# Kernel tuning notes

Hardware: AMD Instinct MI355X
Metric: run time of the kernel (lower is better)

The kernel has to match this reference:

```python
import jax, jax.numpy as jnp
import numpy as np

THRESH = 0.5
MARGIN = 0.1
SCALE_POS = 2.0
SCALE_NEG = 40.0
EPSILON = 1e-5


def setup_inputs() -> dict:
    key = jax.random.key(0)
    kx, kl = jax.random.split(key)
    B, D, N_CLASSES = 4096, 1024, 256
    x = jax.random.normal(kx, (B, D), dtype=jnp.float32)
    # L2-normalize embeddings (standard for multi-similarity loss; keeps sim in [-1, 1])
    x = x / jnp.linalg.norm(x, axis=1, keepdims=True)
    labels = jax.random.randint(kl, (B,), 0, N_CLASSES, dtype=jnp.int64)
    return {"x": x, "labels": labels}


def reference(x, labels):
    B = x.shape[0]
    sim = jnp.matmul(x, x.T)  # [B, B]

    eye = jnp.eye(B, dtype=bool)
    same = labels[:, None] == labels[None, :]
    pos_mask = same & ~eye                      # positives excl. self
    neg_mask = ~same                            # negatives
    pos_valid = pos_mask & (sim < 1.0 - EPSILON)  # pos_pair_ after < 1-eps filter

    # per-row hardest stats (inf/-inf where empty)
    min_pos = jnp.min(jnp.where(pos_valid, sim, jnp.inf), axis=1)   # min over pos_pair_
    max_neg = jnp.max(jnp.where(neg_mask, sim, -jnp.inf), axis=1)   # max over neg_pair_

    # mined pairs
    neg_keep = neg_mask & (sim + MARGIN > min_pos[:, None])
    pos_keep = pos_valid & (sim - MARGIN < max_neg[:, None])

    has_row = (pos_valid.any(axis=1) & neg_mask.any(axis=1)
               & pos_keep.any(axis=1) & neg_keep.any(axis=1))

    pos_sum = jnp.sum(jnp.where(pos_keep, jnp.exp(-SCALE_POS * (sim - THRESH)), 0.0), axis=1)
    neg_sum = jnp.sum(jnp.where(neg_keep, jnp.exp(SCALE_NEG * (sim - THRESH)), 0.0), axis=1)

    pos_loss = jnp.log1p(pos_sum) / SCALE_POS
    neg_loss = jnp.log1p(neg_sum) / SCALE_NEG

    row_loss = jnp.where(has_row, pos_loss + neg_loss, 0.0)
    return jnp.sum(row_loss) / B
```

## Files before the change

kernel.cpp:

```cpp
#include <hip/hip_runtime.h>
#include <hip/hip_bf16.h>
#include <math.h>
#include <stdint.h>


#define THRESH    0.5f
#define MARGIN    0.1f
#define SCALE_POS 2.0f
#define SCALE_NEG 40.0f
#define POS_CAP   (1.0f - 1e-5f)

typedef __bf16 bf16x8 __attribute__((ext_vector_type(8)));
typedef float  f32x4  __attribute__((ext_vector_type(4)));

__device__ __forceinline__ uint16_t f2bf(float f) {
  union { float f; uint32_t u; } v; v.f = f;
  uint32_t u = v.u;
  u += 0x7FFFu + ((u >> 16) & 1u);
  return (uint16_t)(u >> 16);
}

__device__ __forceinline__ uint32_t fenc(float f) {
  union { float f; uint32_t u; } v; v.f = f;
  return (v.u & 0x80000000u) ? ~v.u : (v.u ^ 0x80000000u);
}
__device__ __forceinline__ float fdec(uint32_t k) {
  union { float f; uint32_t u; } v;
  v.u = (k & 0x80000000u) ? (k ^ 0x80000000u) : ~k;
  return v.f;
}

__global__ __launch_bounds__(256) void cvt_bf16_kernel(
    const float* __restrict__ x, uint16_t* __restrict__ y, int n) {
  int i = (blockIdx.x * 256 + threadIdx.x) * 4;
  if (i + 3 < n) {
    float4 v = *(const float4*)(x + i);
    ushort4 o;
    o.x = f2bf(v.x); o.y = f2bf(v.y); o.z = f2bf(v.z); o.w = f2bf(v.w);
    *(ushort4*)(y + i) = o;
  }
}

#if defined(__has_builtin)
#if __has_builtin(__builtin_amdgcn_global_load_lds)
#define HAVE_GLL 1
#endif
#endif

__device__ __forceinline__ void stage16(const uint16_t* g, uint16_t* lds_wave_base, int lane) {
#ifdef HAVE_GLL
  __builtin_amdgcn_global_load_lds(
      (const __attribute__((address_space(1))) void*)g,
      (__attribute__((address_space(3))) void*)lds_wave_base, 16, 0, 0);
#else
  *(uint4*)(lds_wave_base + lane * 8) = *(const uint4*)g;
#endif
}

__global__ __launch_bounds__(256) void simgemm_kernel(
    const uint16_t* __restrict__ X, const int* __restrict__ labels,
    float* __restrict__ C, uint32_t* __restrict__ gmin, uint32_t* __restrict__ gmax,
    int B, int D) {
  __shared__ __align__(16) uint16_t sT[2][2][128 * 64];
  __shared__ int slabR[128];
  __shared__ int slabC[128];

  const int nblk = B >> 7;
  const int nb   = nblk * (nblk + 1) / 2;

  int t = blockIdx.x;
  if ((nb & 7) == 0) {
    const int cpx = nb >> 3;
    t = (t % 8) * cpx + t / 8;
  }
  int bi = 0;
  while (t >= nblk - bi) { t -= nblk - bi; ++bi; }
  const int bj = bi + t;
  const int bm = bi * 128;
  const int bn = bj * 128;

  const int tid  = threadIdx.x;
  const int wave = tid >> 6;
  const int lane = tid & 63;
  const int waveM = wave >> 1, waveN = wave & 1;

  if (tid < 128) slabR[tid] = labels[bm + tid];
  else           slabC[tid - 128] = labels[bn + tid - 128];

  const uint16_t* gA = X + (size_t)bm * D;
  const uint16_t* gB = X + (size_t)bn * D;

  int srcOff[4];
#pragma unroll
  for (int s = 0; s < 4; ++s) {
    const int idx = s * 256 + tid;
    const int row = idx >> 3;
    const int cb  = ((idx & 7) << 4) ^ ((row & 7) << 4);
    srcOff[s] = row * D + (cb >> 1);
  }

  const int fr = lane & 15;
  const int fq = lane >> 4;
  const int sw = (fr & 7) << 4;

  f32x4 acc[4][4] = {};

  const int NT = D >> 6;

#pragma unroll
  for (int s = 0; s < 4; ++s) {
    uint16_t* dA = &sT[0][0][0] + (s * 256 + wave * 64) * 8;
    uint16_t* dB = &sT[0][1][0] + (s * 256 + wave * 64) * 8;
    stage16(gA + srcOff[s], dA, lane);
    stage16(gB + srcOff[s], dB, lane);
  }
  __syncthreads();

  int cur = 0;
  for (int kt = 0; kt < NT; ++kt) {
    if (kt + 1 < NT) {
      const int k0 = (kt + 1) << 6;
#pragma unroll
      for (int s = 0; s < 4; ++s) {
        uint16_t* dA = &sT[cur ^ 1][0][0] + (s * 256 + wave * 64) * 8;
        uint16_t* dB = &sT[cur ^ 1][1][0] + (s * 256 + wave * 64) * 8;
        stage16(gA + srcOff[s] + k0, dA, lane);
        stage16(gB + srcOff[s] + k0, dB, lane);
      }
    }

    const char* tA = (const char*)&sT[cur][0][0];
    const char* tB = (const char*)&sT[cur][1][0];
#pragma unroll
    for (int kk = 0; kk < 2; ++kk) {
      const int cbyte = (kk * 64 + fq * 16) ^ sw;
      bf16x8 af[4], bfv[4];
#pragma unroll
      for (int mt = 0; mt < 4; ++mt) {
        const int rowa = waveM * 64 + mt * 16 + fr;
        af[mt] = *(const bf16x8*)(tA + rowa * 128 + cbyte);
      }
#pragma unroll
      for (int nt = 0; nt < 4; ++nt) {
        const int rowb = waveN * 64 + nt * 16 + fr;
        bfv[nt] = *(const bf16x8*)(tB + rowb * 128 + cbyte);
      }
#pragma unroll
      for (int mt = 0; mt < 4; ++mt)
#pragma unroll
        for (int nt = 0; nt < 4; ++nt)
          acc[mt][nt] = __builtin_amdgcn_mfma_f32_16x16x32_bf16(
              af[mt], bfv[nt], acc[mt][nt], 0, 0, 0);
    }

    __syncthreads();
    cur ^= 1;
  }

#pragma unroll
  for (int mt = 0; mt < 4; ++mt) {
#pragma unroll
    for (int nt = 0; nt < 4; ++nt) {
      const int col = bn + waveN * 64 + nt * 16 + fr;
#pragma unroll
      for (int r = 0; r < 4; ++r) {
        const int row = bm + waveM * 64 + mt * 16 + fq * 4 + r;
        C[(size_t)row * B + col] = acc[mt][nt][r];
      }
    }
  }

  if (bi != bj) {
#pragma unroll
    for (int mt = 0; mt < 4; ++mt) {
#pragma unroll
      for (int nt = 0; nt < 4; ++nt) {
        const int col  = bn + waveN * 64 + nt * 16 + fr;
        const int rowb = bm + waveM * 64 + mt * 16 + fq * 4;
        *(f32x4*)(C + (size_t)col * B + rowb) = acc[mt][nt];
      }
    }
  }

  const float INF = __builtin_inff();

  int lr[4][4];
#pragma unroll
  for (int mt = 0; mt < 4; ++mt)
#pragma unroll
    for (int r = 0; r < 4; ++r)
      lr[mt][r] = slabR[waveM * 64 + mt * 16 + fq * 4 + r];
  int lc[4];
#pragma unroll
  for (int nt = 0; nt < 4; ++nt) lc[nt] = slabC[waveN * 64 + nt * 16 + fr];

  {
    float rmin[4][4], rmax[4][4];
#pragma unroll
    for (int mt = 0; mt < 4; ++mt)
#pragma unroll
      for (int r = 0; r < 4; ++r) { rmin[mt][r] = INF; rmax[mt][r] = -INF; }

#pragma unroll
    for (int mt = 0; mt < 4; ++mt) {
#pragma unroll
      for (int nt = 0; nt < 4; ++nt) {
        const int gcol = bn + waveN * 64 + nt * 16 + fr;
#pragma unroll
        for (int r = 0; r < 4; ++r) {
          const int grow = bm + waveM * 64 + mt * 16 + fq * 4 + r;
          const float s = acc[mt][nt][r];
          if (lr[mt][r] == lc[nt]) {
            if (grow != gcol && s < POS_CAP) rmin[mt][r] = fminf(rmin[mt][r], s);
          } else {
            rmax[mt][r] = fmaxf(rmax[mt][r], s);
          }
        }
      }
    }
#pragma unroll
    for (int mt = 0; mt < 4; ++mt)
#pragma unroll
      for (int r = 0; r < 4; ++r) {
#pragma unroll
        for (int m = 1; m < 16; m <<= 1) {
          rmin[mt][r] = fminf(rmin[mt][r], __shfl_xor(rmin[mt][r], m, 64));
          rmax[mt][r] = fmaxf(rmax[mt][r], __shfl_xor(rmax[mt][r], m, 64));
        }
      }
    if (fr == 0) {
#pragma unroll
      for (int mt = 0; mt < 4; ++mt)
#pragma unroll
        for (int r = 0; r < 4; ++r) {
          const int grow = bm + waveM * 64 + mt * 16 + fq * 4 + r;
          if (rmin[mt][r] < INF)  atomicMin(&gmin[grow], fenc(rmin[mt][r]));
          if (rmax[mt][r] > -INF) atomicMax(&gmax[grow], fenc(rmax[mt][r]));
        }
    }
  }

  if (bi != bj) {
    float cmin[4], cmax[4];
#pragma unroll
    for (int nt = 0; nt < 4; ++nt) { cmin[nt] = INF; cmax[nt] = -INF; }

#pragma unroll
    for (int nt = 0; nt < 4; ++nt) {
      const int gcol = bn + waveN * 64 + nt * 16 + fr;
#pragma unroll
      for (int mt = 0; mt < 4; ++mt) {
#pragma unroll
        for (int r = 0; r < 4; ++r) {
          const int grow = bm + waveM * 64 + mt * 16 + fq * 4 + r;
          const float s = acc[mt][nt][r];
          if (lc[nt] == lr[mt][r]) {
            if (grow != gcol && s < POS_CAP) cmin[nt] = fminf(cmin[nt], s);
          } else {
            cmax[nt] = fmaxf(cmax[nt], s);
          }
        }
      }
    }
#pragma unroll
    for (int nt = 0; nt < 4; ++nt) {
#pragma unroll
      for (int m = 16; m < 64; m <<= 1) {
        cmin[nt] = fminf(cmin[nt], __shfl_xor(cmin[nt], m, 64));
        cmax[nt] = fmaxf(cmax[nt], __shfl_xor(cmax[nt], m, 64));
      }
    }
    if (fq == 0) {
#pragma unroll
      for (int nt = 0; nt < 4; ++nt) {
        const int gcol = bn + waveN * 64 + nt * 16 + fr;
        if (cmin[nt] < INF)  atomicMin(&gmin[gcol], fenc(cmin[nt]));
        if (cmax[nt] > -INF) atomicMax(&gmax[gcol], fenc(cmax[nt]));
      }
    }
  }
}

__global__ __launch_bounds__(256) void rowloss_kernel(
    const float* __restrict__ sim, const int* __restrict__ labels,
    const uint32_t* __restrict__ gmin, const uint32_t* __restrict__ gmax,
    float* __restrict__ rowbuf, int B) {
  __shared__ int   slab[4096];
  __shared__ float red[8];

  const int tid  = threadIdx.x;
  const int wave = tid >> 6;
  const int lane = tid & 63;
  const float INF = __builtin_inff();

  for (int tq = tid; tq < (B >> 2); tq += 256)
    ((int4*)slab)[tq] = ((const int4*)labels)[tq];
  __syncthreads();

  const int iters = B >> 10;
  for (int rr = 0; rr < 4; ++rr) {
    const int i = blockIdx.x * 4 + rr;
    const float* row = sim + (size_t)i * B;
    const int li = slab[i];

    const uint32_t kmin = gmin[i], kmax = gmax[i];
    const bool haspos = (kmin != 0xFFFFFFFFu);
    const bool hasneg = (kmax != 0u);
    const float minpos = haspos ? fdec(kmin) : INF;
    const float maxneg = hasneg ? fdec(kmax) : -INF;

    float psum = 0.f, nsum = 0.f;
    for (int it = 0; it < iters; ++it) {
      const int j = it * 1024 + tid * 4;
      float4 v = *(const float4*)(row + j);
      float s4[4] = {v.x, v.y, v.z, v.w};
#pragma unroll
      for (int q = 0; q < 4; ++q) {
        const int jj = j + q;
        const float s = s4[q];
        if (slab[jj] == li) {
          if (jj != i && s < POS_CAP && (s - MARGIN < maxneg))
            psum += __expf(-SCALE_POS * (s - THRESH));
        } else {
          if (s + MARGIN > minpos)
            nsum += __expf(SCALE_NEG * (s - THRESH));
        }
      }
    }

#pragma unroll
    for (int m = 32; m > 0; m >>= 1) {
      psum += __shfl_xor(psum, m, 64);
      nsum += __shfl_xor(nsum, m, 64);
    }
    if (lane == 0) { red[wave] = psum; red[4 + wave] = nsum; }
    __syncthreads();

    if (tid == 0) {
      psum = red[0] + red[1] + red[2] + red[3];
      nsum = red[4] + red[5] + red[6] + red[7];
      const bool has_row = haspos && hasneg && (psum > 0.f) && (nsum > 0.f);
      rowbuf[i] = has_row
          ? (log1pf(psum) * (1.0f / SCALE_POS) + log1pf(nsum) * (1.0f / SCALE_NEG))
          : 0.f;
    }
    __syncthreads();
  }
}

__global__ __launch_bounds__(256) void finalreduce_kernel(
    const float* __restrict__ rowbuf, float* __restrict__ out, int B) {
  __shared__ float red[4];
  const int tid  = threadIdx.x;
  const int wave = tid >> 6;
  const int lane = tid & 63;

  float s = 0.f;
  for (int j = tid * 4; j < B; j += 1024) {
    float4 v = *(const float4*)(rowbuf + j);
    s += v.x + v.y + v.z + v.w;
  }
#pragma unroll
  for (int m = 32; m > 0; m >>= 1) s += __shfl_xor(s, m, 64);
  if (lane == 0) red[wave] = s;
  __syncthreads();
  if (tid == 0)
    out[0] = (red[0] + red[1] + red[2] + red[3]) * (1.0f / (float)B);
}

extern "C" void kernel_launch(void* const* d_in, const int* in_sizes, int n_in,
                              void* d_out, int out_size, void* d_ws, size_t ws_size,
                              hipStream_t stream) {
  const float* x      = (const float*)d_in[0];
  const int*   labels = (const int*)d_in[1];
  float*       out    = (float*)d_out;

  const int B = in_sizes[1];
  const int D = in_sizes[0] / B;

  uint16_t* xbf = (uint16_t*)d_ws;
  size_t xbytes = (((size_t)B * D * 2) + 255) & ~(size_t)255;
  float* sim = (float*)((char*)d_ws + xbytes);
  size_t simbytes = (size_t)B * B * 4;
  float* rowbuf = (float*)((char*)d_ws + xbytes + simbytes);
  uint32_t* gmin = (uint32_t*)((char*)d_ws + xbytes + simbytes + (size_t)B * 4);
  uint32_t* gmax = (uint32_t*)((char*)d_ws + xbytes + simbytes + (size_t)B * 8);

  hipMemsetAsync(gmin, 0xFF, (size_t)B * 4, stream);
  hipMemsetAsync(gmax, 0x00, (size_t)B * 4, stream);

  const int n = B * D;
  cvt_bf16_kernel<<<n / 1024, 256, 0, stream>>>(x, xbf, n);

  const int nblk = B / 128;
  const int nb   = nblk * (nblk + 1) / 2;
  simgemm_kernel<<<nb, 256, 0, stream>>>(xbf, labels, sim, gmin, gmax, B, D);

  rowloss_kernel<<<B / 4, 256, 0, stream>>>(sim, labels, gmin, gmax, rowbuf, B);
  finalreduce_kernel<<<1, 256, 0, stream>>>(rowbuf, out, B);
}
```

Before: 148.1 us.

## Fold memsets and final reduce into kernels, shrink GEMM K-tile, batch rowloss rows

Measured after the change: 205.4 us. 38.7% more time.

```diff
diff --git a/kernel.cpp b/kernel.cpp
--- a/kernel.cpp
+++ b/kernel.cpp
@@ -31,13 +31,23 @@
 }
 
 __global__ __launch_bounds__(256) void cvt_bf16_kernel(
-    const float* __restrict__ x, uint16_t* __restrict__ y, int n) {
-  int i = (blockIdx.x * 256 + threadIdx.x) * 4;
+    const float* __restrict__ x, uint16_t* __restrict__ y, int n,
+    uint32_t* __restrict__ gmin, uint32_t* __restrict__ gmax,
+    uint32_t* __restrict__ cnt, int B) {
+  const int tid = threadIdx.x;
+  int i = (blockIdx.x * 256 + tid) * 4;
   if (i + 3 < n) {
     float4 v = *(const float4*)(x + i);
     ushort4 o;
     o.x = f2bf(v.x); o.y = f2bf(v.y); o.z = f2bf(v.z); o.w = f2bf(v.w);
     *(ushort4*)(y + i) = o;
+  }
+  if (blockIdx.x == 0) {
+    for (int j = tid; j < B; j += 256) {
+      gmin[j] = 0xFFFFFFFFu;
+      gmax[j] = 0u;
+    }
+    if (tid == 0) *cnt = 0u;
   }
 }
 
@@ -61,7 +71,7 @@
     const uint16_t* __restrict__ X, const int* __restrict__ labels,
     float* __restrict__ C, uint32_t* __restrict__ gmin, uint32_t* __restrict__ gmax,
     int B, int D) {
-  __shared__ __align__(16) uint16_t sT[2][2][128 * 64];
+  __shared__ __align__(16) uint16_t sT[2][2][128 * 32];
   __shared__ int slabR[128];
   __shared__ int slabC[128];
 
@@ -90,25 +100,25 @@
   const uint16_t* gA = X + (size_t)bm * D;
   const uint16_t* gB = X + (size_t)bn * D;
 
-  int srcOff[4];
-#pragma unroll
-  for (int s = 0; s < 4; ++s) {
+  int srcOff[2];
+#pragma unroll
+  for (int s = 0; s < 2; ++s) {
     const int idx = s * 256 + tid;
-    const int row = idx >> 3;
-    const int cb  = ((idx & 7) << 4) ^ ((row & 7) << 4);
+    const int row = idx >> 2;
+    const int cb  = ((idx & 3) << 4) ^ ((row & 3) << 4);
     srcOff[s] = row * D + (cb >> 1);
   }
 
   const int fr = lane & 15;
   const int fq = lane >> 4;
-  const int sw = (fr & 7) << 4;
+  const int sw = (fr & 3) << 4;
 
   f32x4 acc[4][4] = {};
 
-  const int NT = D >> 6;
-
-#pragma unroll
-  for (int s = 0; s < 4; ++s) {
+  const int NT = D >> 5;
+
+#pragma unroll
+  for (int s = 0; s < 2; ++s) {
     uint16_t* dA = &sT[0][0][0] + (s * 256 + wave * 64) * 8;
     uint16_t* dB = &sT[0][1][0] + (s * 256 + wave * 64) * 8;
     stage16(gA + srcOff[s], dA, lane);
@@ -119,9 +129,9 @@
   int cur = 0;
   for (int kt = 0; kt < NT; ++kt) {
     if (kt + 1 < NT) {
-      const int k0 = (kt + 1) << 6;
-#pragma unroll
-      for (int s = 0; s < 4; ++s) {
+      const int k0 = (kt + 1) << 5;
+#pragma unroll
+      for (int s = 0; s < 2; ++s) {
         uint16_t* dA = &sT[cur ^ 1][0][0] + (s * 256 + wave * 64) * 8;
         uint16_t* dB = &sT[cur ^ 1][1][0] + (s * 256 + wave * 64) * 8;
         stage16(gA + srcOff[s] + k0, dA, lane);
@@ -131,27 +141,24 @@
 
     const char* tA = (const char*)&sT[cur][0][0];
     const char* tB = (const char*)&sT[cur][1][0];
-#pragma unroll
-    for (int kk = 0; kk < 2; ++kk) {
-      const int cbyte = (kk * 64 + fq * 16) ^ sw;
-      bf16x8 af[4], bfv[4];
-#pragma unroll
-      for (int mt = 0; mt < 4; ++mt) {
-        const int rowa = waveM * 64 + mt * 16 + fr;
-        af[mt] = *(const bf16x8*)(tA + rowa * 128 + cbyte);
-      }
-#pragma unroll
-      for (int nt = 0; nt < 4; ++nt) {
-        const int rowb = waveN * 64 + nt * 16 + fr;
-        bfv[nt] = *(const bf16x8*)(tB + rowb * 128 + cbyte);
-      }
-#pragma unroll
-      for (int mt = 0; mt < 4; ++mt)
-#pragma unroll
-        for (int nt = 0; nt < 4; ++nt)
-          acc[mt][nt] = __builtin_amdgcn_mfma_f32_16x16x32_bf16(
-              af[mt], bfv[nt], acc[mt][nt], 0, 0, 0);
-    }
+    const int cbyte = (fq * 16) ^ sw;
+    bf16x8 af[4], bfv[4];
+#pragma unroll
+    for (int mt = 0; mt < 4; ++mt) {
+      const int rowa = waveM * 64 + mt * 16 + fr;
+      af[mt] = *(const bf16x8*)(tA + rowa * 64 + cbyte);
+    }
+#pragma unroll
+    for (int nt = 0; nt < 4; ++nt) {
+      const int rowb = waveN * 64 + nt * 16 + fr;
+      bfv[nt] = *(const bf16x8*)(tB + rowb * 64 + cbyte);
+    }
+#pragma unroll
+    for (int mt = 0; mt < 4; ++mt)
+#pragma unroll
+      for (int nt = 0; nt < 4; ++nt)
+        acc[mt][nt] = __builtin_amdgcn_mfma_f32_16x16x32_bf16(
+            af[mt], bfv[nt], acc[mt][nt], 0, 0, 0);
 
     __syncthreads();
     cur ^= 1;
@@ -244,7 +251,6 @@
     float cmin[4], cmax[4];
 #pragma unroll
     for (int nt = 0; nt < 4; ++nt) { cmin[nt] = INF; cmax[nt] = -INF; }
-
 #pragma unroll
     for (int nt = 0; nt < 4; ++nt) {
       const int gcol = bn + waveN * 64 + nt * 16 + fr;
@@ -284,9 +290,12 @@
 __global__ __launch_bounds__(256) void rowloss_kernel(
     const float* __restrict__ sim, const int* __restrict__ labels,
     const uint32_t* __restrict__ gmin, const uint32_t* __restrict__ gmax,
-    float* __restrict__ rowbuf, int B) {
+    float* __restrict__ rowbuf, float* __restrict__ out,
+    uint32_t* __restrict__ cnt, int B) {
   __shared__ int   slab[4096];
-  __shared__ float red[8];
+  __shared__ float red[4][8];
+  __shared__ float fred[4];
+  __shared__ int   isLast;
 
   const int tid  = threadIdx.x;
   const int wave = tid >> 6;
@@ -297,75 +306,94 @@
     ((int4*)slab)[tq] = ((const int4*)labels)[tq];
   __syncthreads();
 
+  const int i0 = blockIdx.x * 4;
+
+  float minpos[4], maxneg[4];
+  bool  haspos[4], hasneg[4];
+  int   li[4];
+#pragma unroll
+  for (int r = 0; r < 4; ++r) {
+    const uint32_t km = gmin[i0 + r], kx = gmax[i0 + r];
+    haspos[r] = (km != 0xFFFFFFFFu);
+    hasneg[r] = (kx != 0u);
+    minpos[r] = haspos[r] ? fdec(km) : INF;
+    maxneg[r] = hasneg[r] ? fdec(kx) : -INF;
+    li[r] = slab[i0 + r];
+  }
+
+  float ps[4] = {}, ns[4] = {};
   const int iters = B >> 10;
-  for (int rr = 0; rr < 4; ++rr) {
-    const int i = blockIdx.x * 4 + rr;
-    const float* row = sim + (size_t)i * B;
-    const int li = slab[i];
-
-    const uint32_t kmin = gmin[i], kmax = gmax[i];
-    const bool haspos = (kmin != 0xFFFFFFFFu);
-    const bool hasneg = (kmax != 0u);
-    const float minpos = haspos ? fdec(kmin) : INF;
-    const float maxneg = hasneg ? fdec(kmax) : -INF;
-
-    float psum = 0.f, nsum = 0.f;
-    for (int it = 0; it < iters; ++it) {
-      const int j = it * 1024 + tid * 4;
-      float4 v = *(const float4*)(row + j);
-      float s4[4] = {v.x, v.y, v.z, v.w};
+  for (int it = 0; it < iters; ++it) {
+    const int j = it * 1024 + tid * 4;
+    float4 v[4];
+#pragma unroll
+    for (int r = 0; r < 4; ++r)
+      v[r] = *(const float4*)(sim + (size_t)(i0 + r) * B + j);
+#pragma unroll
+    for (int r = 0; r < 4; ++r) {
+      const int i = i0 + r;
+      float s4[4] = {v[r].x, v[r].y, v[r].z, v[r].w};
 #pragma unroll
       for (int q = 0; q < 4; ++q) {
         const int jj = j + q;
         const float s = s4[q];
-        if (slab[jj] == li) {
-          if (jj != i && s < POS_CAP && (s - MARGIN < maxneg))
-            psum += __expf(-SCALE_POS * (s - THRESH));
+        if (slab[jj] == li[r]) {
+          if (jj != i && s < POS_CAP && (s - MARGIN < maxneg[r]))
+            ps[r] += __expf(-SCALE_POS * (s - THRESH));
         } else {
-          if (s + MARGIN > minpos)
-            nsum += __expf(SCALE_NEG * (s - THRESH));
+          if (s + MARGIN > minpos[r])
+            ns[r] += __expf(SCALE_NEG * (s - THRESH));
         }
       }
     }
-
+  }
+
+#pragma unroll
+  for (int r = 0; r < 4; ++r) {
 #pragma unroll
     for (int m = 32; m > 0; m >>= 1) {
-      psum += __shfl_xor(psum, m, 64);
-      nsum += __shfl_xor(nsum, m, 64);
-    }
-    if (lane == 0) { red[wave] = psum; red[4 + wave] = nsum; }
+      ps[r] += __shfl_xor(ps[r], m, 64);
+      ns[r] += __shfl_xor(ns[r], m, 64);
+    }
+  }
+  if (lane == 0) {
+#pragma unroll
+    for (int r = 0; r < 4; ++r) { red[wave][r] = ps[r]; red[wave][4 + r] = ns[r]; }
+  }
+  __syncthreads();
+
+  if (tid < 4) {
+    const int r = tid;
+    const float P = red[0][r] + red[1][r] + red[2][r] + red[3][r];
+    const float N = red[0][4 + r] + red[1][4 + r] + red[2][4 + r] + red[3][4 + r];
+    const bool has_row = haspos[r] && hasneg[r] && (P > 0.f) && (N > 0.f);
+    rowbuf[i0 + r] = has_row
+        ? (log1pf(P) * (1.0f / SCALE_POS) + log1pf(N) * (1.0f / SCALE_NEG))
+        : 0.f;
+  }
+  __threadfence();
+  __syncthreads();
+
+  if (tid == 0) {
+    const uint32_t v = atomicAdd(cnt, 1u);
+    isLast = (v == (uint32_t)(gridDim.x - 1)) ? 1 : 0;
+  }
+  __syncthreads();
+
+  if (isLast) {
+    __threadfence();
+    float s = 0.f;
+    for (int j = tid * 4; j < B; j += 1024) {
+      float4 v = *(const float4*)(rowbuf + j);
+      s += v.x + v.y + v.z + v.w;
+    }
+#pragma unroll
+    for (int m = 32; m > 0; m >>= 1) s += __shfl_xor(s, m, 64);
+    if (lane == 0) fred[wave] = s;
     __syncthreads();
-
-    if (tid == 0) {
-      psum = red[0] + red[1] + red[2] + red[3];
-      nsum = red[4] + red[5] + red[6] + red[7];
-      const bool has_row = haspos && hasneg && (psum > 0.f) && (nsum > 0.f);
-      rowbuf[i] = has_row
-          ? (log1pf(psum) * (1.0f / SCALE_POS) + log1pf(nsum) * (1.0f / SCALE_NEG))
-          : 0.f;
-    }
-    __syncthreads();
-  }
-}
-
-__global__ __launch_bounds__(256) void finalreduce_kernel(
-    const float* __restrict__ rowbuf, float* __restrict__ out, int B) {
-  __shared__ float red[4];
-  const int tid  = threadIdx.x;
-  const int wave = tid >> 6;
-  const int lane = tid & 63;
-
-  float s = 0.f;
-  for (int j = tid * 4; j < B; j += 1024) {
-    float4 v = *(const float4*)(rowbuf + j);
-    s += v.x + v.y + v.z + v.w;
-  }
-#pragma unroll
-  for (int m = 32; m > 0; m >>= 1) s += __shfl_xor(s, m, 64);
-  if (lane == 0) red[wave] = s;
-  __syncthreads();
-  if (tid == 0)
-    out[0] = (red[0] + red[1] + red[2] + red[3]) * (1.0f / (float)B);
+    if (tid == 0)
+      out[0] = (fred[0] + fred[1] + fred[2] + fred[3]) * (1.0f / (float)B);
+  }
 }
 
 extern "C" void kernel_launch(void* const* d_in, const int* in_sizes, int n_in,
@@ -378,24 +406,21 @@
   const int B = in_sizes[1];
   const int D = in_sizes[0] / B;
 
-  uint16_t* xbf = (uint16_t*)d_ws;
-  size_t xbytes = (((size_t)B * D * 2) + 255) & ~(size_t)255;
-  float* sim = (float*)((char*)d_ws + xbytes);
-  size_t simbytes = (size_t)B * B * 4;
-  float* rowbuf = (float*)((char*)d_ws + xbytes + simbytes);
-  uint32_t* gmin = (uint32_t*)((char*)d_ws + xbytes + simbytes + (size_t)B * 4);
-  uint32_t* gmax = (uint32_t*)((char*)d_ws + xbytes + simbytes + (size_t)B * 8);
-
-  hipMemsetAsync(gmin, 0xFF, (size_t)B * 4, stream);
-  hipMemsetAsync(gmax, 0x00, (size_t)B * 4, stream);
+  char* ws = (char*)d_ws;
+  uint16_t* xbf = (uint16_t*)ws;       ws += (((size_t)B * D * 2) + 255) & ~(size_t)255;
+  float* sim = (float*)ws;             ws += (size_t)B * B * 4;
+  uint32_t* gmin = (uint32_t*)ws;      ws += (size_t)B * 4;
+  uint32_t* gmax = (uint32_t*)ws;      ws += (size_t)B * 4;
+  float* rowbuf = (float*)ws;          ws += (size_t)B * 4;
+  uint32_t* cnt = (uint32_t*)ws;       ws += 256;
 
   const int n = B * D;
-  cvt_bf16_kernel<<<n / 1024, 256, 0, stream>>>(x, xbf, n);
+  cvt_bf16_kernel<<<n / 1024, 256, 0, stream>>>(x, xbf, n, gmin, gmax, cnt, B);
 
   const int nblk = B / 128;
   const int nb   = nblk * (nblk + 1) / 2;
   simgemm_kernel<<<nb, 256, 0, stream>>>(xbf, labels, sim, gmin, gmax, B, D);
 
-  rowloss_kernel<<<B / 4, 256, 0, stream>>>(sim, labels, gmin, gmax, rowbuf, B);
-  finalreduce_kernel<<<1, 256, 0, stream>>>(rowbuf, out, B);
-}
+  rowloss_kernel<<<B / 4, 256, 0, stream>>>(sim, labels, gmin, gmax,
+                                            rowbuf, out, cnt, B);
+}
```
